# Performance work log

Measured on AMD Instinct MI355X. Metric: run time of the kernel, lower is better.

The kernel has to match this reference:

```python
import jax, jax.numpy as jnp
import numpy as np

T, H, NH, NKV, HD = 4096, 2048, 16, 2, 256
ROT = 64           # partial_rotary_factor 0.25 * head_dim 256
HALF = ROT // 2    # 32 == sum(mrope_section [11, 11, 10])
BASE = 10_000_000.0
EPS = 1e-6
SCALE = HD ** -0.5


def setup_inputs() -> dict:
    key = jax.random.key(0)
    ks = jax.random.split(key, 8)
    s = 0.02
    return {
        "positions": jnp.sort(jax.random.randint(ks[0], (3, T), 0, 4096), axis=-1),
        "hidden": jax.random.normal(ks[1], (T, H), jnp.float32),
        "Wq": jax.random.normal(ks[2], (H, NH * HD * 2), jnp.float32) * s,
        "Wk": jax.random.normal(ks[3], (H, NKV * HD), jnp.float32) * s,
        "Wv": jax.random.normal(ks[4], (H, NKV * HD), jnp.float32) * s,
        "Wo": jax.random.normal(ks[5], (NH * HD, H), jnp.float32) * s,
        "q_norm_w": jax.random.normal(ks[6], (HD,), jnp.float32) * 0.1,
        "k_norm_w": jax.random.normal(ks[7], (HD,), jnp.float32) * 0.1,
    }


def _rms(x, w):
    # GemmaRMSNorm: x / rms * (1 + w), per-head over last dim
    var = jnp.mean(x * x, axis=-1, keepdims=True)
    return x * jax.lax.rsqrt(var + EPS) * (1.0 + w)


def _rope_tables(positions):
    # interleaved MRoPE: freq j uses position axis j % 3 -> counts [11,11,10]
    inv_freq = BASE ** (-jnp.arange(0, ROT, 2, dtype=jnp.float32) / ROT)  # [HALF]
    axis = jnp.arange(HALF) % 3
    pos = positions[axis, :].astype(jnp.float32)   # [HALF, T]
    freqs = pos.T * inv_freq                       # [T, HALF]
    return jnp.cos(freqs), jnp.sin(freqs)


def _apply_rope(x, cos, sin):
    # x: [T, heads, HD]; rotate first ROT dims (neox half-split), rest pass through
    x1, x2 = x[..., :HALF], x[..., HALF:ROT]
    c, s = cos[:, None, :], sin[:, None, :]
    return jnp.concatenate([x1 * c - x2 * s, x2 * c + x1 * s, x[..., ROT:]], axis=-1)


def reference(positions, hidden, Wq, Wk, Wv, Wo, q_norm_w, k_norm_w):
    qg = (hidden @ Wq).reshape(T, NH, 2 * HD)
    q, gate = qg[..., :HD], qg[..., HD:]          # chunk(2, dim=-1)
    k = (hidden @ Wk).reshape(T, NKV, HD)
    v = (hidden @ Wv).reshape(T, NKV, HD)
    q = _rms(q, q_norm_w)
    k = _rms(k, k_norm_w)
    cos, sin = _rope_tables(positions)
    q = _apply_rope(q, cos, sin)
    k = _apply_rope(k, cos, sin)
    # GQA causal attention: group 16 Q heads over 2 KV heads
    g = NH // NKV
    q4 = q.reshape(T, NKV, g, HD)
    scores = jnp.einsum('qkgd,tkd->kgqt', q4, k) * SCALE   # [NKV, g, T, T]
    mask = jnp.tril(jnp.ones((T, T), dtype=bool))
    scores = jnp.where(mask[None, None], scores, -jnp.inf)
    probs = jax.nn.softmax(scores, axis=-1)
    o = jnp.einsum('kgqt,tkd->qkgd', probs, v).reshape(T, NH, HD)
    o = o * jax.nn.sigmoid(gate)                   # per-head output gating
    return o.reshape(T, NH * HD) @ Wo
```

## Files before the change

kernel.cpp:

```cpp
#include <hip/hip_runtime.h>
#include <hip/hip_bf16.h>


#define T_SZ 4096
#define H_SZ 2048
#define NH_SZ 16
#define NKV_SZ 2
#define HD_SZ 256
#define ATT_SCALE 0.0625f
#define SOFT_M 18.0f
#define EPS_ 1e-6f

typedef __attribute__((ext_vector_type(8))) short bf16x8;
typedef __attribute__((ext_vector_type(4))) float f32x4;

#define MFMA16(a, b, c) __builtin_amdgcn_mfma_f32_16x16x32_bf16((a), (b), (c), 0, 0, 0)

__device__ __forceinline__ void async16(const void* g, void* l) {
  __builtin_amdgcn_global_load_lds((const __attribute__((address_space(1))) void*)g,
                                   (__attribute__((address_space(3))) void*)l,
                                   16, 0, 0);
}

__device__ __forceinline__ float to_f(float x) { return x; }
__device__ __forceinline__ float to_f(__hip_bfloat16 x) { return __bfloat162float(x); }

union BfBits { __hip_bfloat16 h; unsigned short u; };

__device__ __forceinline__ unsigned short bf16_bits(__hip_bfloat16 h) {
  BfBits t; t.h = h; return t.u;
}

__device__ __forceinline__ unsigned pack_hilo(float v) {
  __hip_bfloat16 hi = __float2bfloat16(v);
  float rem = v - __bfloat162float(hi);
  __hip_bfloat16 lo = __float2bfloat16(rem);
  return (unsigned)bf16_bits(hi) | ((unsigned)bf16_bits(lo) << 16);
}

__global__ __launch_bounds__(256) void rope_table(const int* __restrict__ pos,
                                                  float2* __restrict__ tab) {
  int id = blockIdx.x * 256 + threadIdx.x;
  int t = id >> 5, i = id & 31;
  float p = (float)pos[(i % 3) * T_SZ + t];
  float fr = p * exp2f((float)i * (-0.72667177075661f));
  float c, s;
  sincosf(fr, &s, &c);
  tab[id] = make_float2(c, s);
}

__global__ __launch_bounds__(256) void cast_f32_bf16(const float* __restrict__ in,
                                                     __hip_bfloat16* __restrict__ out,
                                                     int n4) {
  int i = blockIdx.x * 256 + threadIdx.x;
  if (i >= n4) return;
  float4 v = ((const float4*)in)[i];
  union { __hip_bfloat16 h[4]; uint2 u; } t;
  t.h[0] = __float2bfloat16(v.x);
  t.h[1] = __float2bfloat16(v.y);
  t.h[2] = __float2bfloat16(v.z);
  t.h[3] = __float2bfloat16(v.w);
  ((uint2*)out)[i] = t.u;
}

template <typename TIN>
__global__ __launch_bounds__(256) void transpose_cast(const TIN* __restrict__ in,
                                                      __hip_bfloat16* __restrict__ out,
                                                      int R, int C) {
  __shared__ TIN tile[32][33];
  int c0 = blockIdx.x * 32, r0 = blockIdx.y * 32;
  int tx = threadIdx.x & 31, ty = threadIdx.x >> 5;
#pragma unroll
  for (int i = 0; i < 32; i += 8)
    tile[ty + i][tx] = in[(long)(r0 + ty + i) * C + c0 + tx];
  __syncthreads();
#pragma unroll
  for (int i = 0; i < 32; i += 8)
    out[(long)(c0 + ty + i) * R + r0 + tx] = __float2bfloat16(to_f(tile[tx][ty + i]));
}

__global__ __launch_bounds__(512) void gemm_qg2(const __hip_bfloat16* __restrict__ A,
                                                const __hip_bfloat16* __restrict__ BT,
                                                unsigned* __restrict__ qpk,
                                                __hip_bfloat16* __restrict__ gate,
                                                const float2* __restrict__ tab,
                                                const float* __restrict__ qw) {
  __shared__ __align__(16) __hip_bfloat16 As[4][8192];
  __shared__ __align__(16) __hip_bfloat16 Bs[4][8192];
  const int tid = threadIdx.x, wid = tid >> 6, lane = tid & 63;
  const int lo = lane & 15, quad = lane >> 4;
  const int wm = (wid >> 2) * 128, wn = (wid & 3) * 64;
  const int wnx = wid & 3;
  const int wg = blockIdx.x + blockIdx.y * 8;
  const int xcd = wg & 7, i_ = wg >> 3;
  const long n0 = (long)(xcd * 4 + (i_ & 3)) * 256;
  const long m0 = (long)(i_ >> 2) * 256;
  const int K = 2048;

  const int r0_ = tid >> 2;
  const int kc0 = (tid & 3) ^ ((tid >> 3) & 3);
  const __hip_bfloat16* sA0 = A + (m0 + r0_) * K + kc0 * 8;
  const __hip_bfloat16* sA1 = A + (m0 + r0_ + 128) * K + kc0 * 8;
  const __hip_bfloat16* sB0 = BT + (n0 + r0_) * K + kc0 * 8;
  const __hip_bfloat16* sB1 = BT + (n0 + r0_ + 128) * K + kc0 * 8;

  const int xq = (lo >> 1) & 3;
  const int aoff = (wm + lo) * 32 + ((quad ^ xq) * 8);
  const int boff = (wn + lo) * 32 + ((quad ^ xq) * 8);

  const f32x4 z4 = {0.f, 0.f, 0.f, 0.f};
  f32x4 acc[8][4];
#pragma unroll
  for (int fr = 0; fr < 8; ++fr)
#pragma unroll
    for (int fn = 0; fn < 4; ++fn) acc[fr][fn] = z4;

#define QG_STAGE(buf, kt) do {                                   \
    const int off_ = (kt) * 32;                                  \
    async16(sA0 + off_, &As[buf][tid * 8]);                      \
    async16(sA1 + off_, &As[buf][tid * 8 + 4096]);               \
    async16(sB0 + off_, &Bs[buf][tid * 8]);                      \
    async16(sB1 + off_, &Bs[buf][tid * 8 + 4096]);               \
  } while (0)

#define QG_COMPUTE(buf_) do {                                    \
    bf16x8 af[8], bq[4];                                         \
    _Pragma("unroll")                                            \
    for (int fr = 0; fr < 8; ++fr)                               \
      af[fr] = *(const bf16x8*)(&As[buf_][aoff + fr * 512]);     \
    _Pragma("unroll")                                            \
    for (int fn = 0; fn < 4; ++fn)                               \
      bq[fn] = *(const bf16x8*)(&Bs[buf_][boff + fn * 512]);     \
    __builtin_amdgcn_s_setprio(1);                               \
    _Pragma("unroll")                                            \
    for (int fr = 0; fr < 8; ++fr)                               \
      _Pragma("unroll")                                          \
      for (int fn = 0; fn < 4; ++fn)                             \
        acc[fr][fn] = MFMA16(af[fr], bq[fn], acc[fr][fn]);       \
    __builtin_amdgcn_s_setprio(0);                               \
  } while (0)

  QG_STAGE(0, 0); QG_STAGE(1, 1); QG_STAGE(2, 2);
  for (int kt = 0; kt < 61; ++kt) {
    asm volatile("s_waitcnt vmcnt(8)" ::: "memory");
    __builtin_amdgcn_s_barrier();
    __builtin_amdgcn_sched_barrier(0);
    QG_STAGE((kt + 3) & 3, kt + 3);
    __builtin_amdgcn_sched_barrier(0);
    QG_COMPUTE(kt & 3);
  }
  asm volatile("s_waitcnt vmcnt(8)" ::: "memory");
  __builtin_amdgcn_s_barrier();
  __builtin_amdgcn_sched_barrier(0);
  QG_COMPUTE(1);
  asm volatile("s_waitcnt vmcnt(4)" ::: "memory");
  __builtin_amdgcn_s_barrier();
  __builtin_amdgcn_sched_barrier(0);
  QG_COMPUTE(2);
  asm volatile("s_waitcnt vmcnt(0)" ::: "memory");
  __builtin_amdgcn_s_barrier();
  __builtin_amdgcn_sched_barrier(0);
  QG_COMPUTE(3);
#undef QG_STAGE
#undef QG_COMPUTE

  const int head = (int)(n0 >> 9);
  const bool isq = ((n0 >> 8) & 1) == 0;
  if (!isq) {
#pragma unroll
    for (int fr = 0; fr < 8; ++fr)
#pragma unroll
      for (int fn = 0; fn < 4; ++fn)
#pragma unroll
        for (int rr = 0; rr < 4; ++rr) {
          long row = m0 + wm + fr * 16 + quad * 4 + rr;
          int c = wn + fn * 16 + lo;
          gate[(row * NH_SZ + head) * 256 + c] = __float2bfloat16(acc[fr][fn][rr]);
        }
  } else {
    __syncthreads();
    float* red = (float*)&As[0][0];
#pragma unroll
    for (int fr = 0; fr < 8; ++fr)
#pragma unroll
      for (int rr = 0; rr < 4; ++rr) {
        float p = 0.f;
#pragma unroll
        for (int fn = 0; fn < 4; ++fn) { float x = acc[fr][fn][rr]; p += x * x; }
#pragma unroll
        for (int off = 1; off < 16; off <<= 1) p += __shfl_xor(p, off);
        if (lo == 0) red[(wm + fr * 16 + quad * 4 + rr) * 4 + wnx] = p;
      }
    __syncthreads();
    float wq4[4];
#pragma unroll
    for (int fn = 0; fn < 4; ++fn) wq4[fn] = 1.0f + qw[wn + fn * 16 + lo];
#pragma unroll
    for (int fr = 0; fr < 8; ++fr)
#pragma unroll
      for (int rr = 0; rr < 4; ++rr) {
        int rl = wm + fr * 16 + quad * 4 + rr;
        float4 rv = *(const float4*)&red[rl * 4];
        float sc = rsqrtf((rv.x + rv.y + rv.z + rv.w) * (1.0f / 256.0f) + EPS_);
        float v[4];
#pragma unroll
        for (int fn = 0; fn < 4; ++fn) v[fn] = acc[fr][fn][rr] * sc * wq4[fn];
        long row = m0 + rl;
        if (wnx == 0) {
#pragma unroll
          for (int fnp = 0; fnp < 2; ++fnp) {
            int i = fnp * 16 + lo;
            float2 cs = tab[row * 32 + i];
            float x1 = v[fnp], x2 = v[fnp + 2];
            v[fnp] = x1 * cs.x - x2 * cs.y;
            v[fnp + 2] = x2 * cs.x + x1 * cs.y;
          }
        }
        long base = (row * NH_SZ + head) * 256;
#pragma unroll
        for (int fn = 0; fn < 4; ++fn)
          qpk[base + wn + fn * 16 + lo] = pack_hilo(v[fn]);
      }
  }
}

__global__ __launch_bounds__(256) void gemm_kv(const __hip_bfloat16* __restrict__ A,
                                               const __hip_bfloat16* __restrict__ BT,
                                               float* __restrict__ kf,
                                               __hip_bfloat16* __restrict__ vraw,
                                               int M, int N, int K) {
  __shared__ __align__(16) __hip_bfloat16 As[128 * 32];
  __shared__ __align__(16) __hip_bfloat16 Bs[128 * 32];
  const int tid = threadIdx.x;
  const int wid = tid >> 6, lane = tid & 63;
  const int lo = lane & 15, quad = lane >> 4;
  const int wq = blockIdx.x + blockIdx.y * 8;
  const int xcd = wq & 7, idx = wq >> 3;
  const long n0 = (long)xcd * 128;
  const long m0 = (long)idx * 128;
  const int wm = (wid >> 1) * 64, wn = (wid & 1) * 64;
  const f32x4 z4 = {0.f, 0.f, 0.f, 0.f};
  f32x4 acc[4][4];
#pragma unroll
  for (int i = 0; i < 4; ++i)
#pragma unroll
    for (int j = 0; j < 4; ++j) acc[i][j] = z4;

  const int cf0 = tid, cf1 = 256 + tid;
  const int r0_ = cf0 >> 2, c0_ = (cf0 & 3) * 8;
  const int r1_ = cf1 >> 2, c1_ = (cf1 & 3) * 8;
  const __hip_bfloat16* a0 = A + (m0 + r0_) * K + c0_;
  const __hip_bfloat16* a1 = A + (m0 + r1_) * K + c1_;
  const __hip_bfloat16* b0 = BT + (n0 + r0_) * K + c0_;
  const __hip_bfloat16* b1 = BT + (n0 + r1_) * K + c1_;

  for (int k0 = 0; k0 < K; k0 += 32) {
    async16(a0 + k0, As + cf0 * 8);
    async16(a1 + k0, As + cf1 * 8);
    async16(b0 + k0, Bs + cf0 * 8);
    async16(b1 + k0, Bs + cf1 * 8);
    __syncthreads();
    bf16x8 af[4], bfv[4];
#pragma unroll
    for (int i = 0; i < 4; ++i)
      af[i] = *(const bf16x8*)(As + (wm + i * 16 + lo) * 32 + quad * 8);
#pragma unroll
    for (int i = 0; i < 4; ++i)
      bfv[i] = *(const bf16x8*)(Bs + (wn + i * 16 + lo) * 32 + quad * 8);
#pragma unroll
    for (int i = 0; i < 4; ++i)
#pragma unroll
      for (int j = 0; j < 4; ++j) acc[i][j] = MFMA16(af[i], bfv[j], acc[i][j]);
    __syncthreads();
  }
#pragma unroll
  for (int i = 0; i < 4; ++i)
#pragma unroll
    for (int j = 0; j < 4; ++j)
#pragma unroll
      for (int r = 0; r < 4; ++r) {
        long row = m0 + wm + i * 16 + quad * 4 + r;
        long col = n0 + wn + j * 16 + lo;
        float v = acc[i][j][r];
        if (col < 512)
          kf[row * 512 + col] = v;
        else
          vraw[row * 512 + (col - 512)] = __float2bfloat16(v);
      }
}

__global__ __launch_bounds__(256) void v_swizzle(const __hip_bfloat16* __restrict__ vraw,
                                                 __hip_bfloat16* __restrict__ vsw) {
  const int ktt = blockIdx.x, kvh = blockIdx.y, tid = threadIdx.x;
  __shared__ __hip_bfloat16 L[64 * 264];
#pragma unroll
  for (int it = 0; it < 8; ++it) {
    int cf = it * 256 + tid;
    int kv = cf >> 5, d0 = (cf & 31) * 8;
    *(uint4*)&L[kv * 264 + d0] =
        *(const uint4*)&vraw[(((long)ktt * 64 + kv) * NKV_SZ + kvh) * 256 + d0];
  }
  __syncthreads();
#pragma unroll
  for (int it = 0; it < 8; ++it) {
    int cf = it * 256 + tid;
    int c = cf >> 8, d = cf & 255;
    union { __hip_bfloat16 h[8]; uint4 u; } t;
#pragma unroll
    for (int e = 0; e < 8; ++e) t.h[e] = L[(c * 8 + e) * 264 + d];
    *(uint4*)&vsw[((long)kvh * 64 + ktt) * 16384 + (long)(c * 256 + d) * 8] = t.u;
  }
}

__global__ __launch_bounds__(256) void norm_rope_k(const float* __restrict__ kbuf,
                                                   __hip_bfloat16* __restrict__ ksw,
                                                   const float2* __restrict__ tab,
                                                   const float* __restrict__ kw) {
  const int id = blockIdx.x * 4 + (threadIdx.x >> 6);
  const int lane = threadIdx.x & 63;
  const int kv = id & 1, t = id >> 1;
  const float* ptr = kbuf + ((long)t * NKV_SZ + kv) * 256;
  float4 v = *(const float4*)(ptr + lane * 4);
  float4 wv = *(const float4*)(kw + lane * 4);
  float s2 = v.x * v.x + v.y * v.y + v.z * v.z + v.w * v.w;
#pragma unroll
  for (int o = 32; o > 0; o >>= 1) s2 += __shfl_xor(s2, o);
  float sc = rsqrtf(s2 * (1.0f / 256.0f) + EPS_);
  float n[4];
  n[0] = v.x * sc * (1.0f + wv.x);
  n[1] = v.y * sc * (1.0f + wv.y);
  n[2] = v.z * sc * (1.0f + wv.z);
  n[3] = v.w * sc * (1.0f + wv.w);
  float pr[4];
#pragma unroll
  for (int j = 0; j < 4; ++j) pr[j] = __shfl_xor(n[j], 8);
  float o4[4];
  if (lane < 16) {
    int base_i = (lane & 7) * 4;
#pragma unroll
    for (int j = 0; j < 4; ++j) {
      int i = base_i + j;
      float2 cs = tab[(long)t * 32 + i];
      o4[j] = (lane < 8) ? n[j] * cs.x - pr[j] * cs.y
                         : n[j] * cs.x + pr[j] * cs.y;
    }
  } else {
#pragma unroll
    for (int j = 0; j < 4; ++j) o4[j] = n[j];
  }
  long tt = t >> 5; int r = t & 31;
  int c = lane >> 1, e0 = (lane & 1) * 4;
  union { __hip_bfloat16 h4[4]; uint2 u; } kk;
#pragma unroll
  for (int j = 0; j < 4; ++j) kk.h4[j] = __float2bfloat16(o4[j]);
  *(uint2*)&ksw[(((long)kv * 128 + tt) * 32 + c) * 256 + r * 8 + e0] = kk.u;
}

__global__ __launch_bounds__(256) void attn_kernel(unsigned* __restrict__ Qp,
                                                   const __hip_bfloat16* __restrict__ Ksw,
                                                   const __hip_bfloat16* __restrict__ Vsw,
                                                   const __hip_bfloat16* __restrict__ Gt) {
  const int w = blockIdx.x + blockIdx.y * 64;
  const int xcd = w & 7, j = w >> 3;
  const int h = xcd * 2 + (j & 1);
  const int qt = 63 - (j >> 1);
  const int kvh = h >> 3;
  const int tid = threadIdx.x, wid = tid >> 6, lane = tid & 63;
  const int lo = lane & 15, quad = lane >> 4;
  __shared__ __align__(16) __hip_bfloat16 Ks[32 * 256];
  __shared__ __align__(16) __hip_bfloat16 Vs[4 * 2048];
  __shared__ __align__(16) __hip_bfloat16 Ps[4][16 * 40];

  __hip_bfloat16* myP = &Ps[wid][0];
  const f32x4 z4 = {0.f, 0.f, 0.f, 0.f};
  const int nt = 2 * (qt + 1);

  bf16x8 qh[8], ql[8];
  {
    const unsigned* qp =
        Qp + ((long)(qt * 64 + wid * 16 + lo) * NH_SZ + h) * 256 + quad * 8;
#pragma unroll
    for (int kc = 0; kc < 8; ++kc) {
      uint4 p0 = *(const uint4*)(qp + kc * 32);
      uint4 p1 = *(const uint4*)(qp + kc * 32 + 4);
      bf16x8 a, b;
      a[0] = (short)(p0.x & 0xffff); b[0] = (short)(p0.x >> 16);
      a[1] = (short)(p0.y & 0xffff); b[1] = (short)(p0.y >> 16);
      a[2] = (short)(p0.z & 0xffff); b[2] = (short)(p0.z >> 16);
      a[3] = (short)(p0.w & 0xffff); b[3] = (short)(p0.w >> 16);
      a[4] = (short)(p1.x & 0xffff); b[4] = (short)(p1.x >> 16);
      a[5] = (short)(p1.y & 0xffff); b[5] = (short)(p1.y >> 16);
      a[6] = (short)(p1.z & 0xffff); b[6] = (short)(p1.z >> 16);
      a[7] = (short)(p1.w & 0xffff); b[7] = (short)(p1.w >> 16);
      qh[kc] = a; ql[kc] = b;
    }
  }

  f32x4 acc[16];
#pragma unroll
  for (int od = 0; od < 16; ++od) acc[od] = z4;
  float lsum[4];
#pragma unroll
  for (int r = 0; r < 4; ++r) lsum[r] = 0.f;

  const int qrow_g = qt * 64 + wid * 16 + quad * 4;
  const __hip_bfloat16* kbase = Ksw + (long)kvh * 1048576;
  const __hip_bfloat16* vbase = Vsw + (long)kvh * 1048576;

#pragma unroll
  for (int i = 0; i < 4; ++i) {
    int m = i * 4 + wid;
    async16(kbase + m * 512 + lane * 8, Ks + m * 512 + lane * 8);
    async16(vbase + m * 512 + lane * 8, Vs + m * 512 + lane * 8);
  }
  __syncthreads();

  for (int kt = 0; kt < nt; ++kt) {
    const bool skip = (kt == nt - 1) && (wid < 2);
    f32x4 s[2];
    s[0] = z4; s[1] = z4;
    if (!skip) {
      __builtin_amdgcn_s_setprio(1);
#pragma unroll
      for (int kc = 0; kc < 8; ++kc) {
        bf16x8 ah = qh[kc], al = ql[kc];
#pragma unroll
        for (int ni = 0; ni < 2; ++ni) {
          bf16x8 b = *(const bf16x8*)(Ks + (kc * 4 + quad) * 256 + (ni * 16 + lo) * 8);
          s[ni] = MFMA16(ah, b, s[ni]);
          s[ni] = MFMA16(al, b, s[ni]);
        }
      }
      __builtin_amdgcn_s_setprio(0);
    }
    __syncthreads();
    if (kt + 1 < nt) {
      const __hip_bfloat16* kb = kbase + (long)(kt + 1) * 8192;
#pragma unroll
      for (int i = 0; i < 4; ++i) {
        int m = i * 4 + wid;
        async16(kb + m * 512 + lane * 8, Ks + m * 512 + lane * 8);
      }
    }
    if (!skip) {
      float sv[2][4];
      if (kt >= nt - 2) {
#pragma unroll
        for (int ni = 0; ni < 2; ++ni) {
          int kcol = kt * 32 + ni * 16 + lo;
#pragma unroll
          for (int r = 0; r < 4; ++r) {
            float e = __expf(fmaf(s[ni][r], ATT_SCALE, -SOFT_M));
            sv[ni][r] = (kcol > qrow_g + r) ? 0.f : e;
          }
        }
      } else {
#pragma unroll
        for (int ni = 0; ni < 2; ++ni)
#pragma unroll
          for (int r = 0; r < 4; ++r)
            sv[ni][r] = __expf(fmaf(s[ni][r], ATT_SCALE, -SOFT_M));
      }
#pragma unroll
      for (int r = 0; r < 4; ++r) lsum[r] += sv[0][r] + sv[1][r];
#pragma unroll
      for (int ni = 0; ni < 2; ++ni)
#pragma unroll
        for (int r = 0; r < 4; ++r)
          myP[(quad * 4 + r) * 40 + ni * 16 + lo] = __float2bfloat16(sv[ni][r]);
      bf16x8 ap = *(const bf16x8*)(myP + lo * 40 + quad * 8);
      __builtin_amdgcn_s_setprio(1);
#pragma unroll
      for (int od = 0; od < 16; ++od) {
        bf16x8 bv = *(const bf16x8*)(Vs + quad * 2048 + (od * 16 + lo) * 8);
        acc[od] = MFMA16(ap, bv, acc[od]);
      }
      __builtin_amdgcn_s_setprio(0);
    }
    __syncthreads();
    if (kt + 1 < nt) {
      const __hip_bfloat16* vb = vbase + (long)(kt + 1) * 8192;
#pragma unroll
      for (int i = 0; i < 4; ++i) {
        int m = i * 4 + wid;
        async16(vb + m * 512 + lane * 8, Vs + m * 512 + lane * 8);
      }
    }
  }

  float l_r[4];
#pragma unroll
  for (int r = 0; r < 4; ++r) {
    float su = lsum[r];
#pragma unroll
    for (int off = 1; off < 16; off <<= 1) su += __shfl_xor(su, off);
    l_r[r] = su;
  }
#pragma unroll
  for (int od = 0; od < 16; ++od)
#pragma unroll
    for (int r = 0; r < 4; ++r) {
      int trow = qt * 64 + wid * 16 + quad * 4 + r;
      int col = od * 16 + lo;
      long idx = ((long)trow * NH_SZ + h) * 256 + col;
      float g = __bfloat162float(Gt[idx]);
      float sig = 1.0f / (1.0f + expf(-g));
      float v = (acc[od][r] / l_r[r]) * sig;
      Qp[idx] = pack_hilo(v);
    }
}

__global__ __launch_bounds__(256) void gemm_out(const unsigned* __restrict__ Ap,
                                                const __hip_bfloat16* __restrict__ Bt,
                                                float* __restrict__ C,
                                                int M, int N, int K) {
  __shared__ __align__(16) __hip_bfloat16 Ash[128 * 32];
  __shared__ __align__(16) __hip_bfloat16 Asl[128 * 32];
  __shared__ __align__(16) __hip_bfloat16 Bs[128 * 32];
  const int tid = threadIdx.x;
  const int wid = tid >> 6, lane = tid & 63;
  const int lo = lane & 15, quad = lane >> 4;
  const int wq = blockIdx.x + blockIdx.y * 16;
  const int xcd = wq & 7, idx = wq >> 3;
  const long n0 = (long)(xcd * 2 + (idx & 1)) * 128;
  const long m0 = (long)(idx >> 1) * 128;
  const int wm = (wid >> 1) * 64, wn = (wid & 1) * 64;
  const f32x4 z4 = {0.f, 0.f, 0.f, 0.f};
  f32x4 acc[4][4];
#pragma unroll
  for (int i = 0; i < 4; ++i)
#pragma unroll
    for (int j = 0; j < 4; ++j) acc[i][j] = z4;

  const int cf0 = tid, cf1 = 256 + tid;
  const int br0 = cf0 >> 2, bc0 = (cf0 & 3) * 8;
  const int br1 = cf1 >> 2, bc1 = (cf1 & 3) * 8;
  const __hip_bfloat16* b0 = Bt + (n0 + br0) * K + bc0;
  const __hip_bfloat16* b1 = Bt + (n0 + br1) * K + bc1;

  for (int k0 = 0; k0 < K; k0 += 32) {
    async16(b0 + k0, Bs + cf0 * 8);
    async16(b1 + k0, Bs + cf1 * 8);
#pragma unroll
    for (int it = 0; it < 4; ++it) {
      int c = it * 256 + tid, row = c >> 3, c4 = (c & 7) * 4;
      uint4 p = *(const uint4*)(Ap + (m0 + row) * K + k0 + c4);
      uint2 wh, wl;
      wh.x = (p.x & 0xffff) | ((p.y & 0xffff) << 16);
      wh.y = (p.z & 0xffff) | ((p.w & 0xffff) << 16);
      wl.x = (p.x >> 16) | (p.y & 0xffff0000u);
      wl.y = (p.z >> 16) | (p.w & 0xffff0000u);
      *(uint2*)(Ash + row * 32 + c4) = wh;
      *(uint2*)(Asl + row * 32 + c4) = wl;
    }
    __syncthreads();
    bf16x8 ah[4], al[4], bf[4];
#pragma unroll
    for (int i = 0; i < 4; ++i) {
      ah[i] = *(const bf16x8*)(Ash + (wm + i * 16 + lo) * 32 + quad * 8);
      al[i] = *(const bf16x8*)(Asl + (wm + i * 16 + lo) * 32 + quad * 8);
      bf[i] = *(const bf16x8*)(Bs + (wn + i * 16 + lo) * 32 + quad * 8);
    }
#pragma unroll
    for (int i = 0; i < 4; ++i)
#pragma unroll
      for (int j = 0; j < 4; ++j) {
        acc[i][j] = MFMA16(ah[i], bf[j], acc[i][j]);
        acc[i][j] = MFMA16(al[i], bf[j], acc[i][j]);
      }
    __syncthreads();
  }
#pragma unroll
  for (int i = 0; i < 4; ++i)
#pragma unroll
    for (int j = 0; j < 4; ++j)
#pragma unroll
      for (int r = 0; r < 4; ++r) {
        long row = m0 + wm + i * 16 + quad * 4 + r;
        long col = n0 + wn + j * 16 + lo;
        C[row * N + col] = acc[i][j][r];
      }
}

extern "C" void kernel_launch(void* const* d_in, const int* in_sizes, int n_in,
                              void* d_out, int out_size, void* d_ws, size_t ws_size,
                              hipStream_t stream) {
  (void)in_sizes; (void)n_in; (void)out_size; (void)ws_size;
  const int* positions = (const int*)d_in[0];
  const float* hidden = (const float*)d_in[1];
  const float* Wq = (const float*)d_in[2];
  const float* Wk = (const float*)d_in[3];
  const float* Wv = (const float*)d_in[4];
  const float* Wo = (const float*)d_in[5];
  const float* qw = (const float*)d_in[6];
  const float* kw = (const float*)d_in[7];
  float* out = (float*)d_out;
  char* ws = (char*)d_ws;

  __hip_bfloat16* hid  = (__hip_bfloat16*)(ws + 0);
  __hip_bfloat16* WqT  = (__hip_bfloat16*)(ws + 16777216);
  __hip_bfloat16* WkT  = (__hip_bfloat16*)(ws + 50331648);
  __hip_bfloat16* WvT  = (__hip_bfloat16*)(ws + 52428800);
  float*          qf   = (float*)(ws + 54525952);
  __hip_bfloat16* gate = (__hip_bfloat16*)(ws + 121634816);
  float*          kf   = (float*)(ws + 155189248);
  __hip_bfloat16* vraw = (__hip_bfloat16*)(ws + 163577856);
  __hip_bfloat16* Ksw  = WkT;
  __hip_bfloat16* Vsw  = hid;
  __hip_bfloat16* WoT  = gate;
  unsigned* qpk = (unsigned*)qf;
  float2*   tab = (float2*)out;

  rope_table<<<dim3(512), dim3(256), 0, stream>>>(positions, tab);
  cast_f32_bf16<<<dim3(8192), dim3(256), 0, stream>>>(hidden, hid, 2097152);
  transpose_cast<float><<<dim3(256, 64), dim3(256), 0, stream>>>(Wq, WqT, 2048, 8192);
  transpose_cast<float><<<dim3(16, 64), dim3(256), 0, stream>>>(Wk, WkT, 2048, 512);
  transpose_cast<float><<<dim3(16, 64), dim3(256), 0, stream>>>(Wv, WvT, 2048, 512);
  gemm_qg2<<<dim3(8, 64), dim3(512), 0, stream>>>(hid, WqT, qpk, gate, tab, qw);
  gemm_kv<<<dim3(8, 32), dim3(256), 0, stream>>>(hid, WkT, kf, vraw, 4096, 1024, 2048);
  v_swizzle<<<dim3(64, 2), dim3(256), 0, stream>>>(vraw, Vsw);
  norm_rope_k<<<dim3(2048), dim3(256), 0, stream>>>(kf, Ksw, tab, kw);
  attn_kernel<<<dim3(64, 16), dim3(256), 0, stream>>>(qpk, Ksw, Vsw, gate);
  transpose_cast<float><<<dim3(64, 128), dim3(256), 0, stream>>>(Wo, WoT, 4096, 2048);
  gemm_out<<<dim3(16, 32), dim3(256), 0, stream>>>(qpk, WoT, out, 4096, 2048, 4096);
}
```

Measured before the change: 797.5 us.

## Retile output GEMM to 64x256 blocks with shared A tile across warps

After: 805.3 us. No clear change (+1.0%).

```diff
diff --git a/kernel.cpp b/kernel.cpp
--- a/kernel.cpp
+++ b/kernel.cpp
@@ -514,17 +514,15 @@
                                                 const __hip_bfloat16* __restrict__ Bt,
                                                 float* __restrict__ C,
                                                 int M, int N, int K) {
-  __shared__ __align__(16) __hip_bfloat16 Ash[128 * 32];
-  __shared__ __align__(16) __hip_bfloat16 Asl[128 * 32];
-  __shared__ __align__(16) __hip_bfloat16 Bs[128 * 32];
+  __shared__ __align__(16) __hip_bfloat16 Ash[64 * 32];
+  __shared__ __align__(16) __hip_bfloat16 Asl[64 * 32];
+  __shared__ __align__(16) __hip_bfloat16 Bs[256 * 32];
   const int tid = threadIdx.x;
   const int wid = tid >> 6, lane = tid & 63;
   const int lo = lane & 15, quad = lane >> 4;
-  const int wq = blockIdx.x + blockIdx.y * 16;
-  const int xcd = wq & 7, idx = wq >> 3;
-  const long n0 = (long)(xcd * 2 + (idx & 1)) * 128;
-  const long m0 = (long)(idx >> 1) * 128;
-  const int wm = (wid >> 1) * 64, wn = (wid & 1) * 64;
+  const long n0 = (long)blockIdx.x * 256;
+  const long m0 = (long)blockIdx.y * 64;
+  const int wn = wid * 64;
   const f32x4 z4 = {0.f, 0.f, 0.f, 0.f};
   f32x4 acc[4][4];
 #pragma unroll
@@ -532,17 +530,21 @@
 #pragma unroll
     for (int j = 0; j < 4; ++j) acc[i][j] = z4;
 
-  const int cf0 = tid, cf1 = 256 + tid;
-  const int br0 = cf0 >> 2, bc0 = (cf0 & 3) * 8;
-  const int br1 = cf1 >> 2, bc1 = (cf1 & 3) * 8;
-  const __hip_bfloat16* b0 = Bt + (n0 + br0) * K + bc0;
-  const __hip_bfloat16* b1 = Bt + (n0 + br1) * K + bc1;
+  const __hip_bfloat16* bptr[4];
+#pragma unroll
+  for (int it = 0; it < 4; ++it) {
+    int cf = it * 256 + tid;
+    bptr[it] = Bt + (n0 + (cf >> 2)) * K + (cf & 3) * 8;
+  }
 
   for (int k0 = 0; k0 < K; k0 += 32) {
-    async16(b0 + k0, Bs + cf0 * 8);
-    async16(b1 + k0, Bs + cf1 * 8);
 #pragma unroll
     for (int it = 0; it < 4; ++it) {
+      int cf = it * 256 + tid;
+      async16(bptr[it] + k0, Bs + cf * 8);
+    }
+#pragma unroll
+    for (int it = 0; it < 2; ++it) {
       int c = it * 256 + tid, row = c >> 3, c4 = (c & 7) * 4;
       uint4 p = *(const uint4*)(Ap + (m0 + row) * K + k0 + c4);
       uint2 wh, wl;
@@ -557,8 +559,8 @@
     bf16x8 ah[4], al[4], bf[4];
 #pragma unroll
     for (int i = 0; i < 4; ++i) {
-      ah[i] = *(const bf16x8*)(Ash + (wm + i * 16 + lo) * 32 + quad * 8);
-      al[i] = *(const bf16x8*)(Asl + (wm + i * 16 + lo) * 32 + quad * 8);
+      ah[i] = *(const bf16x8*)(Ash + (i * 16 + lo) * 32 + quad * 8);
+      al[i] = *(const bf16x8*)(Asl + (i * 16 + lo) * 32 + quad * 8);
       bf[i] = *(const bf16x8*)(Bs + (wn + i * 16 + lo) * 32 + quad * 8);
     }
 #pragma unroll
@@ -576,7 +578,7 @@
     for (int j = 0; j < 4; ++j)
 #pragma unroll
       for (int r = 0; r < 4; ++r) {
-        long row = m0 + wm + i * 16 + quad * 4 + r;
+        long row = m0 + i * 16 + quad * 4 + r;
         long col = n0 + wn + j * 16 + lo;
         C[row * N + col] = acc[i][j][r];
       }
@@ -622,5 +624,5 @@
   norm_rope_k<<<dim3(2048), dim3(256), 0, stream>>>(kf, Ksw, tab, kw);
   attn_kernel<<<dim3(64, 16), dim3(256), 0, stream>>>(qpk, Ksw, Vsw, gate);
   transpose_cast<float><<<dim3(64, 128), dim3(256), 0, stream>>>(Wo, WoT, 4096, 2048);
-  gemm_out<<<dim3(16, 32), dim3(256), 0, stream>>>(qpk, WoT, out, 4096, 2048, 4096);
-}
+  gemm_out<<<dim3(8, 64), dim3(256), 0, stream>>>(qpk, WoT, out, 4096, 2048, 4096);
+}
```
